# Optimization experiments

Hardware: AMD Instinct MI355X
Metric: run time of the kernel (lower is better)

Reference implementation:

```python
import jax, jax.numpy as jnp
import numpy as np

KERNEL_SIZE = 9
STRIDE = 1
LN_EPS = 1e-5


def _toeplitz(L, dtype):
    # T[t, l] = 1 iff l - t == STRIDE * i for i in range(KERNEL_SIZE // STRIDE)
    d = jnp.arange(L)[None, :] - jnp.arange(L)[:, None]
    mask = (d >= 0) & (d % STRIDE == 0) & ((d // STRIDE) < (KERNEL_SIZE // STRIDE))
    return mask.astype(dtype)


def setup_inputs() -> dict:
    key = jax.random.key(0)
    ks = jax.random.split(key, 4)
    N, Cin, L, V = 16, 256, 300, 25
    P, Cout = 3, 256
    x = jax.random.normal(ks[0], (N, Cin, L, V), dtype=jnp.float32)
    A = jax.random.uniform(ks[1], (P, V, V), dtype=jnp.float32)
    conv_w = jax.random.normal(ks[2], (Cout * P, Cin), dtype=jnp.float32) * 0.02
    conv_b = jax.random.normal(ks[3], (Cout * P,), dtype=jnp.float32) * 0.02
    ln_gamma = jnp.ones((Cout, 1, V), dtype=jnp.float32)
    ln_beta = jnp.zeros((Cout, 1, V), dtype=jnp.float32)
    edge_importance = jnp.ones((P, V * V), dtype=jnp.float32)
    return {"x": x, "A": A, "conv_w": conv_w, "conv_b": conv_b,
            "ln_gamma": ln_gamma, "ln_beta": ln_beta,
            "edge_importance": edge_importance}


def reference(x, A, conv_w, conv_b, ln_gamma, ln_beta, edge_importance):
    N, Cin, L, V = x.shape
    P = A.shape[0]
    Cout = conv_w.shape[0] // P

    res = x  # in_channels == out_channels and stride == 1 -> identity residual

    # 1x1 conv -> (N, Cout*P, L, V); split into P chunks of Cout along channels
    y = jnp.einsum('nclv,oc->nolv', x, conv_w) + conv_b[None, :, None, None]
    y = y.reshape(N, P, Cout, L, V)  # chunk p == channels [p*Cout:(p+1)*Cout]

    # partitioned graph aggregation with edge importance: (P,V,V) adjacency
    Aw = A * edge_importance.reshape(P, V, V)
    y = jnp.einsum('npclv,pvw->npclw', y, Aw)  # (N, P, Cout, L, V)

    # temporal conv via toeplitz matmul over frame dim L
    T = _toeplitz(L, y.dtype)
    y = jnp.einsum('npclv,lm->npcmv', y, T)  # (N, P, Cout, L, V)

    # sum over partitions -> (N, Cout, L, V)
    y = y.sum(axis=1)

    # LayerNorm over (C, V) per (n, l), affine params shaped (Cout, 1, V)
    mu = jnp.mean(y, axis=(1, 3), keepdims=True)
    var = jnp.var(y, axis=(1, 3), keepdims=True)
    y = (y - mu) * jax.lax.rsqrt(var + LN_EPS)
    y = y * ln_gamma[None] + ln_beta[None]
    y = jax.nn.relu(y)

    # residual add, final ReLU (dropout rate 0.0 -> identity)
    return jax.nn.relu(y + res)
```

## Files before the change

### kernel.cpp

```cpp
#include <hip/hip_runtime.h>

#define NN 16
#define CIN 256
#define COUT 256
#define LL 300
#define VV 25
#define VP 28
#define PP 3
#define KS 9
#define KK 768
#define MM (NN*LL*VV)
#define MPAD 120064
#define MBLK 938
#define XCDS 8
#define NLP 150
#define LPX 19
#define GWID (2*MBLK)
#define GPX 235

typedef float floatx4 __attribute__((ext_vector_type(4)));
typedef short short8 __attribute__((ext_vector_type(8)));

__device__ __forceinline__ unsigned short f2bf(float f) {
    unsigned u = __builtin_bit_cast(unsigned, f);
    u += 0x7fff + ((u >> 16) & 1);
    return (unsigned short)(u >> 16);
}
__device__ __forceinline__ float bf2f(unsigned short h) {
    unsigned u = ((unsigned)h) << 16;
    return __builtin_bit_cast(float, u);
}
__device__ __forceinline__ void gl2lds16(const void* g, void* l) {
    __builtin_amdgcn_global_load_lds(
        (const __attribute__((address_space(1))) void*)g,
        (__attribute__((address_space(3))) void*)l, 16, 0, 0);
}
__device__ __forceinline__ int div25(int x) {
    return (x * 5243) >> 17;
}

__global__ __launch_bounds__(256) void k_prep(
    const float* __restrict__ A, const float* __restrict__ conv_w,
    const float* __restrict__ conv_b, const float* __restrict__ ei,
    unsigned short* __restrict__ w2t, float* __restrict__ b2t,
    unsigned short* __restrict__ xa)
{
    const int t = blockIdx.x * 256 + threadIdx.x;
    const int nthr = gridDim.x * 256;
    for (int idx = t; idx < COUT * KK; idx += nthr) {
        int c = idx / KK, k = idx % KK, p = k >> 8, ci = k & 255;
        w2t[idx] = f2bf(conv_w[(p * COUT + c) * CIN + ci]);
    }
    for (int idx = t; idx < COUT * VV; idx += nthr) {
        int c = idx / VV, w = idx % VV;
        float s = 0.f;
        for (int p = 0; p < PP; ++p) {
            float cs = 0.f;
            for (int v = 0; v < VV; ++v) {
                int a = (p * VV + v) * VV + w;
                cs += A[a] * ei[a];
            }
            s += conv_b[p * COUT + c] * cs;
        }
        b2t[w * COUT + c] = s;
    }
    for (int idx = t; idx < (MPAD - MM) * KK; idx += nthr)
        xa[(size_t)MM * KK + idx] = 0;
}

__global__ __launch_bounds__(256) void k_agg(
    const float* __restrict__ x, const float* __restrict__ A,
    const float* __restrict__ ei, unsigned short* __restrict__ xa)
{
    __shared__ float AwL[PP * VV * VP];
    __shared__ float xL[CIN * VV];
    const int l = blockIdx.x, n = blockIdx.y, t = threadIdx.x;
    for (int idx = t; idx < PP * VV * VV; idx += 256) {
        int pv = idx / VV, w = idx % VV;
        AwL[pv * VP + w] = A[idx] * ei[idx];
    }
    const size_t base_nl = (size_t)n * (CIN * LL * VV) + (size_t)l * VV;
    #pragma unroll
    for (int k = 0; k < VV; ++k) {
        const int idx = k * 256 + t;
        const int ci = div25(idx);
        const int v = idx - ci * 25;
        xL[idx] = x[base_nl + (size_t)ci * (LL * VV) + v];
    }
    __syncthreads();

    float xv[VV];
    #pragma unroll
    for (int v = 0; v < VV; ++v) xv[v] = xL[t * VV + v];

    const size_t mrow = (size_t)(n * LL + l) * VV;
    #pragma unroll
    for (int p = 0; p < PP; ++p) {
        float acc[VV];
        #pragma unroll
        for (int w = 0; w < VV; ++w) acc[w] = 0.f;
        #pragma unroll
        for (int v = 0; v < VV; ++v) {
            const float xvv = xv[v];
            const float* ar = &AwL[(p * VV + v) * VP];
            #pragma unroll
            for (int wq = 0; wq < 24; wq += 4) {
                const float4 f = *(const float4*)(ar + wq);
                acc[wq + 0] += xvv * f.x; acc[wq + 1] += xvv * f.y;
                acc[wq + 2] += xvv * f.z; acc[wq + 3] += xvv * f.w;
            }
            acc[24] += xvv * ar[24];
        }
        #pragma unroll
        for (int w = 0; w < VV; ++w)
            xa[(mrow + w) * KK + p * CIN + t] = f2bf(acc[w]);
    }
}

__global__ __launch_bounds__(256) void k_gemm(
    const unsigned short* __restrict__ xa,
    const unsigned short* __restrict__ w2t,
    unsigned short* __restrict__ z)
{
    __shared__ __align__(16) unsigned short As[128 * 32];
    __shared__ __align__(16) unsigned short Bs[128 * 32];
    const int bid = blockIdx.x;
    const int g = bid & (XCDS - 1), sidx = bid >> 3;
    const int wid = g * GPX + sidx;
    if (wid >= GWID) return;
    const int m0 = (wid >> 1) * 128, c0 = (wid & 1) * 128;
    const int t = threadIdx.x, wv = t >> 6, ln = t & 63;

    floatx4 acc[4][4];
    #pragma unroll
    for (int i = 0; i < 4; ++i)
        #pragma unroll
        for (int j = 0; j < 4; ++j)
            acc[i][j] = (floatx4){0.f, 0.f, 0.f, 0.f};

    const int srow = wv * 32 + (ln >> 2);
    const int scol = (ln & 3) * 8;
    const int mw = (wv >> 1) * 64, nw = (wv & 1) * 64;
    const int frow = ln & 15, fcol = (ln >> 4) * 8;

    for (int kt = 0; kt < KK / 32; ++kt) {
        const int k0 = kt * 32;
        __syncthreads();
        gl2lds16(xa  + (size_t)(m0 + srow)      * KK + k0 + scol, &As[(wv * 32) * 32]);
        gl2lds16(xa  + (size_t)(m0 + srow + 16) * KK + k0 + scol, &As[(wv * 32 + 16) * 32]);
        gl2lds16(w2t + (size_t)(c0 + srow)      * KK + k0 + scol, &Bs[(wv * 32) * 32]);
        gl2lds16(w2t + (size_t)(c0 + srow + 16) * KK + k0 + scol, &Bs[(wv * 32 + 16) * 32]);
        __syncthreads();

        short8 af[4], bf[4];
        #pragma unroll
        for (int i = 0; i < 4; ++i)
            af[i] = *(const short8*)&As[(mw + i * 16 + frow) * 32 + fcol];
        #pragma unroll
        for (int j = 0; j < 4; ++j)
            bf[j] = *(const short8*)&Bs[(nw + j * 16 + frow) * 32 + fcol];
        #pragma unroll
        for (int i = 0; i < 4; ++i)
            #pragma unroll
            for (int j = 0; j < 4; ++j)
                acc[i][j] = __builtin_amdgcn_mfma_f32_16x16x32_bf16(af[i], bf[j], acc[i][j], 0, 0, 0);
    }

    const int q = ln >> 4, cL = ln & 15;
    #pragma unroll
    for (int i = 0; i < 4; ++i) {
        #pragma unroll
        for (int j = 0; j < 4; ++j) {
            #pragma unroll
            for (int r = 0; r < 4; ++r) {
                const int m = m0 + mw + i * 16 + q * 4 + r;
                const int c = c0 + nw + j * 16 + cL;
                if (m < MM) z[(size_t)m * COUT + c] = f2bf(acc[i][j][r]);
            }
        }
    }
}

__global__ __launch_bounds__(256) void k_ln(
    const unsigned short* __restrict__ z, const float* __restrict__ x,
    const float* __restrict__ b2t, const float* __restrict__ gamma,
    const float* __restrict__ beta, float* __restrict__ out)
{
    __shared__ __align__(16) float Y[2 * VV * COUT];
    __shared__ float red[4][4];
    __shared__ float stats[4];

    const int b = blockIdx.x;
    const int g = b & (XCDS - 1);
    const int r = b >> 3;
    const int li = r % LPX;
    const int n  = r / LPX;
    const int lp = g * LPX + li;
    if (lp >= NLP) return;
    const int l0 = lp * 2;
    const int t = threadIdx.x;

    float s10 = 0.f, s20 = 0.f, s11 = 0.f, s21 = 0.f;
    const size_t zrow0 = (size_t)(n * LL) * (VV * COUT);

    #pragma unroll
    for (int i = 0; i < 4; ++i) {
        const int vs = t + 256 * i;
        if (i < 3 || t < 32) {
            float f[10][8];
            #pragma unroll
            for (int j = 0; j < 10; ++j) {
                const int lr = l0 - 8 + j;
                if (lr >= 0) {
                    const short8 rv = *(const short8*)(z + zrow0 + (size_t)lr * (VV * COUT) + vs * 8);
                    #pragma unroll
                    for (int k = 0; k < 8; ++k) f[j][k] = bf2f((unsigned short)rv[k]);
                } else {
                    #pragma unroll
                    for (int k = 0; k < 8; ++k) f[j][k] = 0.f;
                }
            }
            const float cnt0 = (float)(((l0     < 8) ? l0     : 8) + 1);
            const float cnt1 = (float)(((l0 + 1 < 8) ? l0 + 1 : 8) + 1);
            const float4 ba = *(const float4*)(b2t + vs * 8);
            const float4 bb = *(const float4*)(b2t + vs * 8 + 4);
            const float bv[8] = {ba.x, ba.y, ba.z, ba.w, bb.x, bb.y, bb.z, bb.w};
            float y0[8], y1[8];
            #pragma unroll
            for (int k = 0; k < 8; ++k) {
                float smid = f[1][k];
                #pragma unroll
                for (int j = 2; j < 9; ++j) smid += f[j][k];
                const float a = smid + f[0][k] + cnt0 * bv[k];
                const float c = smid + f[9][k] + cnt1 * bv[k];
                y0[k] = a; y1[k] = c;
                s10 += a; s20 += a * a;
                s11 += c; s21 += c * c;
            }
            *(float4*)&Y[vs * 8]                 = (float4){y0[0], y0[1], y0[2], y0[3]};
            *(float4*)&Y[vs * 8 + 4]             = (float4){y0[4], y0[5], y0[6], y0[7]};
            *(float4*)&Y[VV * COUT + vs * 8]     = (float4){y1[0], y1[1], y1[2], y1[3]};
            *(float4*)&Y[VV * COUT + vs * 8 + 4] = (float4){y1[4], y1[5], y1[6], y1[7]};
        }
    }

    #pragma unroll
    for (int off = 32; off; off >>= 1) {
        s10 += __shfl_down(s10, off);
        s20 += __shfl_down(s20, off);
        s11 += __shfl_down(s11, off);
        s21 += __shfl_down(s21, off);
    }
    const int wid = t >> 6, lane = t & 63;
    if (lane == 0) { red[wid][0] = s10; red[wid][1] = s20; red[wid][2] = s11; red[wid][3] = s21; }
    __syncthreads();
    if (t == 0) {
        float S1 = 0.f, S2 = 0.f, T1 = 0.f, T2 = 0.f;
        #pragma unroll
        for (int w2 = 0; w2 < 4; ++w2) { S1 += red[w2][0]; S2 += red[w2][1]; T1 += red[w2][2]; T2 += red[w2][3]; }
        const float inv = 1.f / (COUT * VV);
        float mu = S1 * inv, var = S2 * inv - mu * mu;
        stats[0] = mu; stats[1] = rsqrtf(var + 1e-5f);
        mu = T1 * inv; var = T2 * inv - mu * mu;
        stats[2] = mu; stats[3] = rsqrtf(var + 1e-5f);
    }
    __syncthreads();

    const float mu0 = stats[0], rsd0 = stats[1], mu1 = stats[2], rsd1 = stats[3];
    const int c = t;
    float val[50];
    #pragma unroll
    for (int f = 0; f < 50; ++f) {
        const int dl = (f >= VV) ? 1 : 0;
        const int v = f - dl * VV;
        const float y = Y[dl * (VV * COUT) + v * COUT + c];
        val[f] = (y - (dl ? mu1 : mu0)) * (dl ? rsd1 : rsd0);
    }
    __syncthreads();
    #pragma unroll
    for (int f = 0; f < 50; f += 2)
        *(float2*)&Y[c * 50 + f] = (float2){val[f], val[f + 1]};
    __syncthreads();

    const size_t base_n = (size_t)n * COUT * (LL * VV) + (size_t)l0 * VV;
    #pragma unroll
    for (int k = 0; k < 25; ++k) {
        const int fi = k * 256 + t;
        const int c2 = div25(fi);
        const int j  = fi - c2 * 25;
        const int f0 = 2 * j;
        const int f1 = f0 + 1;
        const int va = (f0 >= VV) ? (f0 - VV) : f0;
        const int vb = (f1 >= VV) ? (f1 - VV) : f1;
        const float2 yv = *(const float2*)&Y[fi * 2];
        const float ga = gamma[c2 * VV + va], gb2 = gamma[c2 * VV + vb];
        const float bb2 = beta[c2 * VV + va],  bc = beta[c2 * VV + vb];
        const size_t goff = base_n + (size_t)c2 * (LL * VV) + f0;
        const float2 xv = *(const float2*)(x + goff);
        float2 o;
        o.x = fmaxf(fmaxf(yv.x * ga  + bb2, 0.f) + xv.x, 0.f);
        o.y = fmaxf(fmaxf(yv.y * gb2 + bc,  0.f) + xv.y, 0.f);
        *(float2*)(out + goff) = o;
    }
}

extern "C" void kernel_launch(void* const* d_in, const int* in_sizes, int n_in,
                              void* d_out, int out_size, void* d_ws, size_t ws_size,
                              hipStream_t stream) {
    const float* x      = (const float*)d_in[0];
    const float* A      = (const float*)d_in[1];
    const float* conv_w = (const float*)d_in[2];
    const float* conv_b = (const float*)d_in[3];
    const float* gamma  = (const float*)d_in[4];
    const float* beta   = (const float*)d_in[5];
    const float* ei     = (const float*)d_in[6];
    float* out = (float*)d_out;

    char* ws = (char*)d_ws;
    unsigned short* xa  = (unsigned short*)ws;
    unsigned short* z   = (unsigned short*)(ws + 184418304);
    unsigned short* w2t = (unsigned short*)(ws + 245891072);
    float*          b2  = (float*)(ws + 246284288);

    k_prep<<<64, 256, 0, stream>>>(A, conv_w, conv_b, ei, w2t, b2, xa);
    k_agg<<<dim3(LL, NN), 256, 0, stream>>>(x, A, ei, xa);
    k_gemm<<<XCDS * GPX, 256, 0, stream>>>(xa, w2t, z);
    k_ln<<<XCDS * LPX * NN, 256, 0, stream>>>(z, x, b2, gamma, beta, out);
}
```

Before: 520.8 us.

## Process one frame per LayerNorm block to cut LDS and registers

The LayerNorm/temporal-sum kernel now handles one frame per block instead of two. This halves shared memory, shrinks register arrays by keeping packed bf16 loads until summation, and adds a launch-bounds occupancy hint. The gamma/beta/ReLU step moves into the per-channel pass, and the residual x loads are batched ahead of the stores. The cost is that each block no longer shares the 8 overlapping z rows with a neighbouring frame, so z reads go from 10 rows per 2 frames to 9 rows per frame, and global writes become scalar instead of float2.

```diff
diff --git a/kernel.cpp b/kernel.cpp
--- a/kernel.cpp
+++ b/kernel.cpp
@@ -13,8 +13,7 @@
 #define MPAD 120064
 #define MBLK 938
 #define XCDS 8
-#define NLP 150
-#define LPX 19
+#define LX 38
 #define GWID (2*MBLK)
 #define GPX 235
 
@@ -181,126 +180,107 @@
     }
 }
 
-__global__ __launch_bounds__(256) void k_ln(
+__global__ __launch_bounds__(256, 4) void k_ln(
     const unsigned short* __restrict__ z, const float* __restrict__ x,
     const float* __restrict__ b2t, const float* __restrict__ gamma,
     const float* __restrict__ beta, float* __restrict__ out)
 {
-    __shared__ __align__(16) float Y[2 * VV * COUT];
-    __shared__ float red[4][4];
-    __shared__ float stats[4];
+    __shared__ __align__(16) float Y[VV * COUT];
+    __shared__ float red[4][2];
+    __shared__ float stats[2];
 
     const int b = blockIdx.x;
     const int g = b & (XCDS - 1);
     const int r = b >> 3;
-    const int li = r % LPX;
-    const int n  = r / LPX;
-    const int lp = g * LPX + li;
-    if (lp >= NLP) return;
-    const int l0 = lp * 2;
+    const int mi = r % LX;
+    const int n  = r / LX;
+    const int l  = g * LX + mi;
+    if (l >= LL) return;
     const int t = threadIdx.x;
 
-    float s10 = 0.f, s20 = 0.f, s11 = 0.f, s21 = 0.f;
     const size_t zrow0 = (size_t)(n * LL) * (VV * COUT);
+    const float cnt = (float)(((l < 8) ? l : 8) + 1);
+    float s1 = 0.f, s2 = 0.f;
 
     #pragma unroll
     for (int i = 0; i < 4; ++i) {
         const int vs = t + 256 * i;
         if (i < 3 || t < 32) {
-            float f[10][8];
-            #pragma unroll
-            for (int j = 0; j < 10; ++j) {
-                const int lr = l0 - 8 + j;
-                if (lr >= 0) {
-                    const short8 rv = *(const short8*)(z + zrow0 + (size_t)lr * (VV * COUT) + vs * 8);
-                    #pragma unroll
-                    for (int k = 0; k < 8; ++k) f[j][k] = bf2f((unsigned short)rv[k]);
-                } else {
-                    #pragma unroll
-                    for (int k = 0; k < 8; ++k) f[j][k] = 0.f;
-                }
-            }
-            const float cnt0 = (float)(((l0     < 8) ? l0     : 8) + 1);
-            const float cnt1 = (float)(((l0 + 1 < 8) ? l0 + 1 : 8) + 1);
+            short8 rv[9];
+            #pragma unroll
+            for (int j = 0; j < 9; ++j) {
+                const int lr = l - 8 + j;
+                if (lr >= 0)
+                    rv[j] = *(const short8*)(z + zrow0 + (size_t)lr * (VV * COUT) + vs * 8);
+                else
+                    rv[j] = (short8){0, 0, 0, 0, 0, 0, 0, 0};
+            }
             const float4 ba = *(const float4*)(b2t + vs * 8);
             const float4 bb = *(const float4*)(b2t + vs * 8 + 4);
             const float bv[8] = {ba.x, ba.y, ba.z, ba.w, bb.x, bb.y, bb.z, bb.w};
-            float y0[8], y1[8];
+            float y[8];
             #pragma unroll
             for (int k = 0; k < 8; ++k) {
-                float smid = f[1][k];
+                float a = cnt * bv[k];
                 #pragma unroll
-                for (int j = 2; j < 9; ++j) smid += f[j][k];
-                const float a = smid + f[0][k] + cnt0 * bv[k];
-                const float c = smid + f[9][k] + cnt1 * bv[k];
-                y0[k] = a; y1[k] = c;
-                s10 += a; s20 += a * a;
-                s11 += c; s21 += c * c;
-            }
-            *(float4*)&Y[vs * 8]                 = (float4){y0[0], y0[1], y0[2], y0[3]};
-            *(float4*)&Y[vs * 8 + 4]             = (float4){y0[4], y0[5], y0[6], y0[7]};
-            *(float4*)&Y[VV * COUT + vs * 8]     = (float4){y1[0], y1[1], y1[2], y1[3]};
-            *(float4*)&Y[VV * COUT + vs * 8 + 4] = (float4){y1[4], y1[5], y1[6], y1[7]};
+                for (int j = 0; j < 9; ++j)
+                    a += bf2f((unsigned short)rv[j][k]);
+                y[k] = a;
+                s1 += a; s2 += a * a;
+            }
+            *(float4*)&Y[vs * 8]     = (float4){y[0], y[1], y[2], y[3]};
+            *(float4*)&Y[vs * 8 + 4] = (float4){y[4], y[5], y[6], y[7]};
         }
     }
 
     #pragma unroll
     for (int off = 32; off; off >>= 1) {
-        s10 += __shfl_down(s10, off);
-        s20 += __shfl_down(s20, off);
-        s11 += __shfl_down(s11, off);
-        s21 += __shfl_down(s21, off);
+        s1 += __shfl_down(s1, off);
+        s2 += __shfl_down(s2, off);
     }
     const int wid = t >> 6, lane = t & 63;
-    if (lane == 0) { red[wid][0] = s10; red[wid][1] = s20; red[wid][2] = s11; red[wid][3] = s21; }
+    if (lane == 0) { red[wid][0] = s1; red[wid][1] = s2; }
     __syncthreads();
     if (t == 0) {
-        float S1 = 0.f, S2 = 0.f, T1 = 0.f, T2 = 0.f;
-        #pragma unroll
-        for (int w2 = 0; w2 < 4; ++w2) { S1 += red[w2][0]; S2 += red[w2][1]; T1 += red[w2][2]; T2 += red[w2][3]; }
+        float S1 = 0.f, S2 = 0.f;
+        #pragma unroll
+        for (int w2 = 0; w2 < 4; ++w2) { S1 += red[w2][0]; S2 += red[w2][1]; }
         const float inv = 1.f / (COUT * VV);
-        float mu = S1 * inv, var = S2 * inv - mu * mu;
+        const float mu = S1 * inv;
+        const float var = S2 * inv - mu * mu;
         stats[0] = mu; stats[1] = rsqrtf(var + 1e-5f);
-        mu = T1 * inv; var = T2 * inv - mu * mu;
-        stats[2] = mu; stats[3] = rsqrtf(var + 1e-5f);
-    }
-    __syncthreads();
-
-    const float mu0 = stats[0], rsd0 = stats[1], mu1 = stats[2], rsd1 = stats[3];
+    }
+    __syncthreads();
+
+    const float mu = stats[0], rsd = stats[1];
     const int c = t;
-    float val[50];
-    #pragma unroll
-    for (int f = 0; f < 50; ++f) {
-        const int dl = (f >= VV) ? 1 : 0;
-        const int v = f - dl * VV;
-        const float y = Y[dl * (VV * COUT) + v * COUT + c];
-        val[f] = (y - (dl ? mu1 : mu0)) * (dl ? rsd1 : rsd0);
-    }
-    __syncthreads();
-    #pragma unroll
-    for (int f = 0; f < 50; f += 2)
-        *(float2*)&Y[c * 50 + f] = (float2){val[f], val[f + 1]};
-    __syncthreads();
-
-    const size_t base_n = (size_t)n * COUT * (LL * VV) + (size_t)l0 * VV;
-    #pragma unroll
-    for (int k = 0; k < 25; ++k) {
+    const float* gp = gamma + c * VV;
+    const float* bp = beta  + c * VV;
+    float val[VV];
+    #pragma unroll
+    for (int v = 0; v < VV; ++v)
+        val[v] = fmaxf((Y[v * COUT + c] - mu) * rsd * gp[v] + bp[v], 0.f);
+    __syncthreads();
+    #pragma unroll
+    for (int v = 0; v < VV; ++v)
+        Y[c * VV + v] = val[v];
+    __syncthreads();
+
+    const size_t base = (size_t)n * COUT * (LL * VV) + (size_t)l * VV;
+    float xr[VV];
+    #pragma unroll
+    for (int k = 0; k < VV; ++k) {
         const int fi = k * 256 + t;
         const int c2 = div25(fi);
-        const int j  = fi - c2 * 25;
-        const int f0 = 2 * j;
-        const int f1 = f0 + 1;
-        const int va = (f0 >= VV) ? (f0 - VV) : f0;
-        const int vb = (f1 >= VV) ? (f1 - VV) : f1;
-        const float2 yv = *(const float2*)&Y[fi * 2];
-        const float ga = gamma[c2 * VV + va], gb2 = gamma[c2 * VV + vb];
-        const float bb2 = beta[c2 * VV + va],  bc = beta[c2 * VV + vb];
-        const size_t goff = base_n + (size_t)c2 * (LL * VV) + f0;
-        const float2 xv = *(const float2*)(x + goff);
-        float2 o;
-        o.x = fmaxf(fmaxf(yv.x * ga  + bb2, 0.f) + xv.x, 0.f);
-        o.y = fmaxf(fmaxf(yv.y * gb2 + bc,  0.f) + xv.y, 0.f);
-        *(float2*)(out + goff) = o;
+        const int v  = fi - c2 * VV;
+        xr[k] = x[base + (size_t)c2 * (LL * VV) + v];
+    }
+    #pragma unroll
+    for (int k = 0; k < VV; ++k) {
+        const int fi = k * 256 + t;
+        const int c2 = div25(fi);
+        const int v  = fi - c2 * VV;
+        out[base + (size_t)c2 * (LL * VV) + v] = fmaxf(Y[fi] + xr[k], 0.f);
     }
 }
 
@@ -325,5 +305,5 @@
     k_prep<<<64, 256, 0, stream>>>(A, conv_w, conv_b, ei, w2t, b2, xa);
     k_agg<<<dim3(LL, NN), 256, 0, stream>>>(x, A, ei, xa);
     k_gemm<<<XCDS * GPX, 256, 0, stream>>>(xa, w2t, z);
-    k_ln<<<XCDS * LPX * NN, 256, 0, stream>>>(z, x, b2, gamma, beta, out);
-}
+    k_ln<<<XCDS * LX * NN, 256, 0, stream>>>(z, x, b2, gamma, beta, out);
+}
```

After: 508.7 us. 1.02x faster.
